# Kernel tuning notes

Hardware: AMD Instinct MI355X
Metric: run time of the kernel (lower is better)

The kernel has to match this reference:

```python
import jax, jax.numpy as jnp
import numpy as np

N_TOKENS = 16384
HIDDEN = 2048
N_EXPERTS = 256
N_GROUPS = 8
TOPK_GROUPS = 4
TOPK = 8
ROUTE_SCALE = 2.5


def setup_inputs() -> dict:
    key = jax.random.key(0)
    k1, k2, k3 = jax.random.split(key, 3)
    x = jax.random.normal(k1, (N_TOKENS, HIDDEN), dtype=jnp.float32)
    weight = jax.random.normal(k2, (N_EXPERTS, HIDDEN), dtype=jnp.float32) * 0.02
    bias = jax.random.normal(k3, (N_EXPERTS,), dtype=jnp.float32) * 0.02
    return {"x": x, "weight": weight, "bias": bias}


def reference(x, weight, bias):
    # linear scoring: [N, E]
    scores = jnp.einsum("nd,ed->ne", x, weight) + bias
    scores = jax.nn.sigmoid(scores)  # score_func == 'sigmoid'
    original_scores = scores
    # bias is not None -> add bias to routing scores
    scores = scores + bias
    n = x.shape[0]
    # grouped routing: [N, G, E/G]
    scores_g = scores.reshape(n, N_GROUPS, N_EXPERTS // N_GROUPS)
    # bias present -> group score = sum of top-2 per group
    top2_vals, _ = jax.lax.top_k(scores_g, 2)
    group_scores = top2_vals.sum(axis=-1)  # [N, G]
    _, grp_idx = jax.lax.top_k(group_scores, TOPK_GROUPS)  # [N, topk_groups]
    keep = jnp.zeros((n, N_GROUPS), dtype=bool).at[
        jnp.arange(n)[:, None], grp_idx
    ].set(True)
    masked = jnp.where(keep[:, :, None], scores_g, -jnp.inf).reshape(n, N_EXPERTS)
    # final top-k experts over masked scores
    _, indices = jax.lax.top_k(masked, TOPK)  # [N, topk]
    weights = jnp.take_along_axis(original_scores, indices, axis=1)
    # sigmoid -> normalize selected weights
    weights = weights / weights.sum(axis=-1, keepdims=True)
    weights = (weights * ROUTE_SCALE).astype(x.dtype)
    return weights, indices
```

## Files before the change

### kernel.cpp

```cpp
#include <hip/hip_runtime.h>
#include <math.h>

#define NT 16384
#define HID 2048
#define NE 256
#define NG 8
#define TOPG 4
#define TOPKK 8

constexpr int BM = 32;
constexpr int KC = 32;

__global__ __launch_bounds__(256) void score_kernel(
    const float* __restrict__ x, const float* __restrict__ w,
    const float* __restrict__ bias, double* __restrict__ sd)
{
    __shared__ float xs[KC][BM];
    __shared__ float wsm[KC][NE];

    const int tid = threadIdx.x;
    const int tx = tid & 31;
    const int ty = tid >> 5;
    const int m0 = blockIdx.x * BM;

    const int xrow = tid & 31;
    const int xko  = (tid >> 5) * 4;

    const float* wbase = w + (size_t)tid * HID;
    const float* xbase = x + (size_t)(m0 + xrow) * HID + xko;

    double accd[4][8];
#pragma unroll
    for (int mi = 0; mi < 4; mi++)
#pragma unroll
        for (int j = 0; j < 8; j++) accd[mi][j] = 0.0;

    float4 wr[8];
    float4 xr;
#pragma unroll
    for (int q = 0; q < 8; q++) wr[q] = *(const float4*)(wbase + q * 4);
    xr = *(const float4*)(xbase);

    for (int k0 = 0; k0 < HID; k0 += KC) {
        __syncthreads();

#pragma unroll
        for (int q = 0; q < 8; q++) {
            wsm[q * 4 + 0][tid] = wr[q].x;
            wsm[q * 4 + 1][tid] = wr[q].y;
            wsm[q * 4 + 2][tid] = wr[q].z;
            wsm[q * 4 + 3][tid] = wr[q].w;
        }
        xs[xko + 0][xrow] = xr.x;
        xs[xko + 1][xrow] = xr.y;
        xs[xko + 2][xrow] = xr.z;
        xs[xko + 3][xrow] = xr.w;

        if (k0 + KC < HID) {
#pragma unroll
            for (int q = 0; q < 8; q++)
                wr[q] = *(const float4*)(wbase + k0 + KC + q * 4);
            xr = *(const float4*)(xbase + k0 + KC);
        }

        __syncthreads();

        float accf[4][8];

        {
            float4 a  = *(const float4*)&xs[0][ty * 4];
            float4 b0 = *(const float4*)&wsm[0][tx * 4];
            float4 b1 = *(const float4*)&wsm[0][128 + tx * 4];
            float av[4] = {a.x, a.y, a.z, a.w};
            float bv[8] = {b0.x, b0.y, b0.z, b0.w, b1.x, b1.y, b1.z, b1.w};
#pragma unroll
            for (int mi = 0; mi < 4; mi++)
#pragma unroll
                for (int j = 0; j < 8; j++)
                    accf[mi][j] = av[mi] * bv[j];
        }

#pragma unroll
        for (int kk = 1; kk < KC; kk++) {
            float4 a  = *(const float4*)&xs[kk][ty * 4];
            float4 b0 = *(const float4*)&wsm[kk][tx * 4];
            float4 b1 = *(const float4*)&wsm[kk][128 + tx * 4];
            float av[4] = {a.x, a.y, a.z, a.w};
            float bv[8] = {b0.x, b0.y, b0.z, b0.w, b1.x, b1.y, b1.z, b1.w};
#pragma unroll
            for (int mi = 0; mi < 4; mi++)
#pragma unroll
                for (int j = 0; j < 8; j++)
                    accf[mi][j] = fmaf(av[mi], bv[j], accf[mi][j]);
        }

#pragma unroll
        for (int mi = 0; mi < 4; mi++)
#pragma unroll
            for (int j = 0; j < 8; j++) accd[mi][j] += (double)accf[mi][j];
    }

#pragma unroll
    for (int mi = 0; mi < 4; mi++) {
        const size_t row = (size_t)(m0 + ty * 4 + mi) * NE;
#pragma unroll
        for (int j = 0; j < 8; j++) {
            const int n = (j < 4) ? (tx * 4 + j) : (128 + tx * 4 + (j - 4));
            double z = accd[mi][j] + (double)bias[n];
            double s = 1.0 / (1.0 + exp(-z));
            sd[row + n] = s;
        }
    }
}

__global__ __launch_bounds__(256) void route_kernel(
    const double* __restrict__ sd, const float* __restrict__ bias,
    float* __restrict__ wout, float* __restrict__ iout)
{
    const int lane = threadIdx.x & 63;
    const int wid  = threadIdx.x >> 6;
    const int tok  = blockIdx.x * 4 + wid;
    const double* srow = sd + (size_t)tok * NE;
    const int e0 = lane * 4;

    const double NEG = -__builtin_inf();

    double s0 = srow[e0 + 0], s1 = srow[e0 + 1], s2 = srow[e0 + 2], s3 = srow[e0 + 3];
    double sb0 = s0 + (double)bias[e0 + 0];
    double sb1 = s1 + (double)bias[e0 + 1];
    double sb2 = s2 + (double)bias[e0 + 2];
    double sb3 = s3 + (double)bias[e0 + 3];

    double m1 = sb0, m2 = NEG;
    if (sb1 > m1) { m2 = m1; m1 = sb1; } else if (sb1 > m2) m2 = sb1;
    if (sb2 > m1) { m2 = m1; m1 = sb2; } else if (sb2 > m2) m2 = sb2;
    if (sb3 > m1) { m2 = m1; m1 = sb3; } else if (sb3 > m2) m2 = sb3;

#pragma unroll
    for (int mask = 1; mask <= 4; mask <<= 1) {
        double o1 = __shfl_xor(m1, mask);
        double o2 = __shfl_xor(m2, mask);
        double n1 = fmax(m1, o1);
        double n2 = fmax(fmin(m1, o1), fmax(m2, o2));
        m1 = n1; m2 = n2;
    }
    double gs = m1 + m2;

    double g[8];
#pragma unroll
    for (int j = 0; j < 8; j++) g[j] = __shfl(gs, j * 8);

    const int myg = lane >> 3;
    int rank = 0;
#pragma unroll
    for (int j = 0; j < 8; j++)
        rank += (g[j] > g[myg] || (g[j] == g[myg] && j < myg)) ? 1 : 0;
    const bool keep = (rank < TOPG);

    double v0 = keep ? sb0 : NEG;
    double v1 = keep ? sb1 : NEG;
    double v2 = keep ? sb2 : NEG;
    double v3 = keep ? sb3 : NEG;

    double wv[TOPKK];
    int    idx[TOPKK];

#pragma unroll
    for (int r = 0; r < TOPKK; r++) {
        double bvv = v0; int bi = e0;
        if (v1 > bvv) { bvv = v1; bi = e0 + 1; }
        if (v2 > bvv) { bvv = v2; bi = e0 + 2; }
        if (v3 > bvv) { bvv = v3; bi = e0 + 3; }
#pragma unroll
        for (int mask = 1; mask <= 32; mask <<= 1) {
            double ov = __shfl_xor(bvv, mask);
            int    oi = __shfl_xor(bi, mask);
            if (ov > bvv || (ov == bvv && oi < bi)) { bvv = ov; bi = oi; }
        }
        const int sel   = bi & 3;
        const int owner = bi >> 2;
        double cands = (sel == 0) ? s0 : (sel == 1) ? s1 : (sel == 2) ? s2 : s3;
        wv[r]  = __shfl(cands, owner);
        idx[r] = bi;
        if (lane == owner) {
            if (sel == 0) v0 = NEG;
            else if (sel == 1) v1 = NEG;
            else if (sel == 2) v2 = NEG;
            else v3 = NEG;
        }
    }

    double sum = 0.0;
#pragma unroll
    for (int r = 0; r < TOPKK; r++) sum += wv[r];
    const double scale = 2.5 / sum;

    if (lane == 0) {
#pragma unroll
        for (int r = 0; r < TOPKK; r++)
            wout[(size_t)tok * TOPKK + r] = (float)(wv[r] * scale);
#pragma unroll
        for (int r = 0; r < TOPKK; r++)
            iout[(size_t)tok * TOPKK + r] = (float)idx[r];
    }
}

extern "C" void kernel_launch(void* const* d_in, const int* in_sizes, int n_in,
                              void* d_out, int out_size, void* d_ws, size_t ws_size,
                              hipStream_t stream) {
    const float* x = (const float*)d_in[0];
    const float* w = (const float*)d_in[1];
    const float* b = (const float*)d_in[2];

    double* sd = (double*)d_ws;
    float* wout = (float*)d_out;
    float* iout = wout + (size_t)NT * TOPKK;

    score_kernel<<<NT / BM, 256, 0, stream>>>(x, w, b, sd);
    route_kernel<<<NT / 4, 256, 0, stream>>>(sd, b, wout, iout);
}
```

Before: 438.1 us.

## Fuse scoring and routing into one kernel, removing double score buffer

Merges the GEMM-plus-sigmoid kernel and the grouped top-k routing kernel into one kernel. Each 32-lane half-wavefront already holds one token's 256 scores in registers and does the group top-2, group ranking and top-8 selection with shuffles. This removes the 32 MB double-precision score write and re-read plus a second launch. It also halves the K chunk to 16 and drops the register prefetch of the next chunk, so global load latency is no longer hidden behind compute. More double accumulation passes per chunk and extra register pressure could offset part of the saving.

Measured after the change: 507.6 us. 1.16x slower.

```diff
diff --git a/kernel.cpp b/kernel.cpp
--- a/kernel.cpp
+++ b/kernel.cpp
@@ -9,11 +9,12 @@
 #define TOPKK 8
 
 constexpr int BM = 32;
-constexpr int KC = 32;
-
-__global__ __launch_bounds__(256) void score_kernel(
+constexpr int KC = 16;
+
+__global__ __launch_bounds__(256) void score_route_kernel(
     const float* __restrict__ x, const float* __restrict__ w,
-    const float* __restrict__ bias, double* __restrict__ sd)
+    const float* __restrict__ bias,
+    float* __restrict__ wout, float* __restrict__ iout)
 {
     __shared__ float xs[KC][BM];
     __shared__ float wsm[KC][NE];
@@ -23,65 +24,42 @@
     const int ty = tid >> 5;
     const int m0 = blockIdx.x * BM;
 
+    double accd[4][8];
+#pragma unroll
+    for (int mi = 0; mi < 4; mi++)
+#pragma unroll
+        for (int j = 0; j < 8; j++) accd[mi][j] = 0.0;
+
     const int xrow = tid & 31;
-    const int xko  = (tid >> 5) * 4;
-
-    const float* wbase = w + (size_t)tid * HID;
-    const float* xbase = x + (size_t)(m0 + xrow) * HID + xko;
-
-    double accd[4][8];
-#pragma unroll
-    for (int mi = 0; mi < 4; mi++)
-#pragma unroll
-        for (int j = 0; j < 8; j++) accd[mi][j] = 0.0;
-
-    float4 wr[8];
-    float4 xr;
-#pragma unroll
-    for (int q = 0; q < 8; q++) wr[q] = *(const float4*)(wbase + q * 4);
-    xr = *(const float4*)(xbase);
+    const int xkp  = tid >> 5;
 
     for (int k0 = 0; k0 < HID; k0 += KC) {
+        const float* wrow = w + (size_t)tid * HID + k0;
+        float4 wv0 = *(const float4*)(wrow + 0);
+        float4 wv1 = *(const float4*)(wrow + 4);
+        float4 wv2 = *(const float4*)(wrow + 8);
+        float4 wv3 = *(const float4*)(wrow + 12);
+        float2 xv  = *(const float2*)(x + (size_t)(m0 + xrow) * HID + k0 + xkp * 2);
+
         __syncthreads();
 
-#pragma unroll
-        for (int q = 0; q < 8; q++) {
-            wsm[q * 4 + 0][tid] = wr[q].x;
-            wsm[q * 4 + 1][tid] = wr[q].y;
-            wsm[q * 4 + 2][tid] = wr[q].z;
-            wsm[q * 4 + 3][tid] = wr[q].w;
-        }
-        xs[xko + 0][xrow] = xr.x;
-        xs[xko + 1][xrow] = xr.y;
-        xs[xko + 2][xrow] = xr.z;
-        xs[xko + 3][xrow] = xr.w;
-
-        if (k0 + KC < HID) {
-#pragma unroll
-            for (int q = 0; q < 8; q++)
-                wr[q] = *(const float4*)(wbase + k0 + KC + q * 4);
-            xr = *(const float4*)(xbase + k0 + KC);
-        }
+        wsm[ 0][tid] = wv0.x; wsm[ 1][tid] = wv0.y; wsm[ 2][tid] = wv0.z; wsm[ 3][tid] = wv0.w;
+        wsm[ 4][tid] = wv1.x; wsm[ 5][tid] = wv1.y; wsm[ 6][tid] = wv1.z; wsm[ 7][tid] = wv1.w;
+        wsm[ 8][tid] = wv2.x; wsm[ 9][tid] = wv2.y; wsm[10][tid] = wv2.z; wsm[11][tid] = wv2.w;
+        wsm[12][tid] = wv3.x; wsm[13][tid] = wv3.y; wsm[14][tid] = wv3.z; wsm[15][tid] = wv3.w;
+        xs[xkp * 2    ][xrow] = xv.x;
+        xs[xkp * 2 + 1][xrow] = xv.y;
 
         __syncthreads();
 
         float accf[4][8];
-
-        {
-            float4 a  = *(const float4*)&xs[0][ty * 4];
-            float4 b0 = *(const float4*)&wsm[0][tx * 4];
-            float4 b1 = *(const float4*)&wsm[0][128 + tx * 4];
-            float av[4] = {a.x, a.y, a.z, a.w};
-            float bv[8] = {b0.x, b0.y, b0.z, b0.w, b1.x, b1.y, b1.z, b1.w};
-#pragma unroll
-            for (int mi = 0; mi < 4; mi++)
-#pragma unroll
-                for (int j = 0; j < 8; j++)
-                    accf[mi][j] = av[mi] * bv[j];
-        }
-
-#pragma unroll
-        for (int kk = 1; kk < KC; kk++) {
+#pragma unroll
+        for (int mi = 0; mi < 4; mi++)
+#pragma unroll
+            for (int j = 0; j < 8; j++) accf[mi][j] = 0.0f;
+
+#pragma unroll
+        for (int kk = 0; kk < KC; kk++) {
             float4 a  = *(const float4*)&xs[kk][ty * 4];
             float4 b0 = *(const float4*)&wsm[kk][tx * 4];
             float4 b1 = *(const float4*)&wsm[kk][128 + tx * 4];
@@ -100,108 +78,120 @@
             for (int j = 0; j < 8; j++) accd[mi][j] += (double)accf[mi][j];
     }
 
+    const double NEG = -__builtin_inf();
+    const int base = (tid & 63) & 32;
+
+    float bj[8];
+#pragma unroll
+    for (int j = 0; j < 8; j++) {
+        const int n = (j < 4) ? (tx * 4 + j) : (128 + tx * 4 + (j - 4));
+        bj[j] = bias[n];
+    }
+
 #pragma unroll
     for (int mi = 0; mi < 4; mi++) {
-        const size_t row = (size_t)(m0 + ty * 4 + mi) * NE;
+        const int tok = m0 + ty * 4 + mi;
+
+        double sg[8], sb[8];
 #pragma unroll
         for (int j = 0; j < 8; j++) {
-            const int n = (j < 4) ? (tx * 4 + j) : (128 + tx * 4 + (j - 4));
-            double z = accd[mi][j] + (double)bias[n];
+            double z = accd[mi][j] + (double)bj[j];
             double s = 1.0 / (1.0 + exp(-z));
-            sd[row + n] = s;
-        }
-    }
-}
-
-__global__ __launch_bounds__(256) void route_kernel(
-    const double* __restrict__ sd, const float* __restrict__ bias,
-    float* __restrict__ wout, float* __restrict__ iout)
-{
-    const int lane = threadIdx.x & 63;
-    const int wid  = threadIdx.x >> 6;
-    const int tok  = blockIdx.x * 4 + wid;
-    const double* srow = sd + (size_t)tok * NE;
-    const int e0 = lane * 4;
-
-    const double NEG = -__builtin_inf();
-
-    double s0 = srow[e0 + 0], s1 = srow[e0 + 1], s2 = srow[e0 + 2], s3 = srow[e0 + 3];
-    double sb0 = s0 + (double)bias[e0 + 0];
-    double sb1 = s1 + (double)bias[e0 + 1];
-    double sb2 = s2 + (double)bias[e0 + 2];
-    double sb3 = s3 + (double)bias[e0 + 3];
-
-    double m1 = sb0, m2 = NEG;
-    if (sb1 > m1) { m2 = m1; m1 = sb1; } else if (sb1 > m2) m2 = sb1;
-    if (sb2 > m1) { m2 = m1; m1 = sb2; } else if (sb2 > m2) m2 = sb2;
-    if (sb3 > m1) { m2 = m1; m1 = sb3; } else if (sb3 > m2) m2 = sb3;
-
-#pragma unroll
-    for (int mask = 1; mask <= 4; mask <<= 1) {
-        double o1 = __shfl_xor(m1, mask);
-        double o2 = __shfl_xor(m2, mask);
-        double n1 = fmax(m1, o1);
-        double n2 = fmax(fmin(m1, o1), fmax(m2, o2));
-        m1 = n1; m2 = n2;
-    }
-    double gs = m1 + m2;
-
-    double g[8];
-#pragma unroll
-    for (int j = 0; j < 8; j++) g[j] = __shfl(gs, j * 8);
-
-    const int myg = lane >> 3;
-    int rank = 0;
-#pragma unroll
-    for (int j = 0; j < 8; j++)
-        rank += (g[j] > g[myg] || (g[j] == g[myg] && j < myg)) ? 1 : 0;
-    const bool keep = (rank < TOPG);
-
-    double v0 = keep ? sb0 : NEG;
-    double v1 = keep ? sb1 : NEG;
-    double v2 = keep ? sb2 : NEG;
-    double v3 = keep ? sb3 : NEG;
-
-    double wv[TOPKK];
-    int    idx[TOPKK];
-
-#pragma unroll
-    for (int r = 0; r < TOPKK; r++) {
-        double bvv = v0; int bi = e0;
-        if (v1 > bvv) { bvv = v1; bi = e0 + 1; }
-        if (v2 > bvv) { bvv = v2; bi = e0 + 2; }
-        if (v3 > bvv) { bvv = v3; bi = e0 + 3; }
-#pragma unroll
-        for (int mask = 1; mask <= 32; mask <<= 1) {
-            double ov = __shfl_xor(bvv, mask);
-            int    oi = __shfl_xor(bi, mask);
-            if (ov > bvv || (ov == bvv && oi < bi)) { bvv = ov; bi = oi; }
-        }
-        const int sel   = bi & 3;
-        const int owner = bi >> 2;
-        double cands = (sel == 0) ? s0 : (sel == 1) ? s1 : (sel == 2) ? s2 : s3;
-        wv[r]  = __shfl(cands, owner);
-        idx[r] = bi;
-        if (lane == owner) {
-            if (sel == 0) v0 = NEG;
-            else if (sel == 1) v1 = NEG;
-            else if (sel == 2) v2 = NEG;
-            else v3 = NEG;
-        }
-    }
-
-    double sum = 0.0;
-#pragma unroll
-    for (int r = 0; r < TOPKK; r++) sum += wv[r];
-    const double scale = 2.5 / sum;
-
-    if (lane == 0) {
-#pragma unroll
-        for (int r = 0; r < TOPKK; r++)
-            wout[(size_t)tok * TOPKK + r] = (float)(wv[r] * scale);
-#pragma unroll
-        for (int r = 0; r < TOPKK; r++)
-            iout[(size_t)tok * TOPKK + r] = (float)idx[r];
+            sg[j] = s;
+            sb[j] = s + (double)bj[j];
+        }
+
+        double m1lo = sb[0], m2lo = NEG;
+        if (sb[1] > m1lo) { m2lo = m1lo; m1lo = sb[1]; } else if (sb[1] > m2lo) m2lo = sb[1];
+        if (sb[2] > m1lo) { m2lo = m1lo; m1lo = sb[2]; } else if (sb[2] > m2lo) m2lo = sb[2];
+        if (sb[3] > m1lo) { m2lo = m1lo; m1lo = sb[3]; } else if (sb[3] > m2lo) m2lo = sb[3];
+        double m1hi = sb[4], m2hi = NEG;
+        if (sb[5] > m1hi) { m2hi = m1hi; m1hi = sb[5]; } else if (sb[5] > m2hi) m2hi = sb[5];
+        if (sb[6] > m1hi) { m2hi = m1hi; m1hi = sb[6]; } else if (sb[6] > m2hi) m2hi = sb[6];
+        if (sb[7] > m1hi) { m2hi = m1hi; m1hi = sb[7]; } else if (sb[7] > m2hi) m2hi = sb[7];
+
+#pragma unroll
+        for (int mask = 1; mask <= 4; mask <<= 1) {
+            double o1 = __shfl_xor(m1lo, mask);
+            double o2 = __shfl_xor(m2lo, mask);
+            double n1 = fmax(m1lo, o1);
+            double n2 = fmax(fmin(m1lo, o1), fmax(m2lo, o2));
+            m1lo = n1; m2lo = n2;
+            o1 = __shfl_xor(m1hi, mask);
+            o2 = __shfl_xor(m2hi, mask);
+            n1 = fmax(m1hi, o1);
+            n2 = fmax(fmin(m1hi, o1), fmax(m2hi, o2));
+            m1hi = n1; m2hi = n2;
+        }
+        const double gs_lo = m1lo + m2lo;
+        const double gs_hi = m1hi + m2hi;
+
+        double g[8];
+#pragma unroll
+        for (int q = 0; q < 4; q++) {
+            g[q]     = __shfl(gs_lo, base + 8 * q);
+            g[4 + q] = __shfl(gs_hi, base + 8 * q);
+        }
+
+        const int glo = tx >> 3;
+        const int ghi = 4 + glo;
+        int rank_lo = 0, rank_hi = 0;
+#pragma unroll
+        for (int q = 0; q < 8; q++) {
+            rank_lo += (g[q] > g[glo] || (g[q] == g[glo] && q < glo)) ? 1 : 0;
+            rank_hi += (g[q] > g[ghi] || (g[q] == g[ghi] && q < ghi)) ? 1 : 0;
+        }
+        const bool keep_lo = (rank_lo < TOPG);
+        const bool keep_hi = (rank_hi < TOPG);
+
+        double v[8];
+#pragma unroll
+        for (int j = 0; j < 8; j++)
+            v[j] = ((j < 4) ? keep_lo : keep_hi) ? sb[j] : NEG;
+
+        double wv[TOPKK];
+        int    idx[TOPKK];
+
+#pragma unroll
+        for (int r = 0; r < TOPKK; r++) {
+            double bv = v[0]; int bi = tx * 4;
+#pragma unroll
+            for (int j = 1; j < 8; j++) {
+                const int ej = (j < 4) ? (tx * 4 + j) : (128 + tx * 4 + (j - 4));
+                if (v[j] > bv) { bv = v[j]; bi = ej; }
+            }
+#pragma unroll
+            for (int mask = 1; mask <= 16; mask <<= 1) {
+                double ov = __shfl_xor(bv, mask);
+                int    oi = __shfl_xor(bi, mask);
+                if (ov > bv || (ov == bv && oi < bi)) { bv = ov; bi = oi; }
+            }
+            const int tx_o = (bi & 127) >> 2;
+            const int slot = (bi < 128) ? (bi & 3) : (4 + (bi & 3));
+            double mysig = sg[0];
+#pragma unroll
+            for (int j = 1; j < 8; j++)
+                if (j == slot) mysig = sg[j];
+            wv[r]  = __shfl(mysig, base + tx_o);
+            idx[r] = bi;
+#pragma unroll
+            for (int j = 0; j < 8; j++)
+                if (tx == tx_o && j == slot) v[j] = NEG;
+        }
+
+        double sum = 0.0;
+#pragma unroll
+        for (int r = 0; r < TOPKK; r++) sum += wv[r];
+        const double scale = 2.5 / sum;
+
+        if (tx == 0) {
+#pragma unroll
+            for (int r = 0; r < TOPKK; r++)
+                wout[(size_t)tok * TOPKK + r] = (float)(wv[r] * scale);
+#pragma unroll
+            for (int r = 0; r < TOPKK; r++)
+                iout[(size_t)tok * TOPKK + r] = (float)idx[r];
+        }
     }
 }
 
@@ -212,10 +202,8 @@
     const float* w = (const float*)d_in[1];
     const float* b = (const float*)d_in[2];
 
-    double* sd = (double*)d_ws;
     float* wout = (float*)d_out;
     float* iout = wout + (size_t)NT * TOPKK;
 
-    score_kernel<<<NT / BM, 256, 0, stream>>>(x, w, b, sd);
-    route_kernel<<<NT / 4, 256, 0, stream>>>(sd, b, wout, iout);
+    score_route_kernel<<<NT / BM, 256, 0, stream>>>(x, w, b, wout, iout);
 }
```
